# Optimization experiments

Hardware: AMD Instinct MI355X
Metric: run time of the kernel (lower is better)

## Reference

```python
import jax, jax.numpy as jnp
import numpy as np

N = 8192      # nodes
IN_FEATS = 128
OUT_FEATS = 64
DEG = 16      # avg degree for random edges
NEG_SLOPE = 0.01  # nn.LeakyReLU default


def setup_inputs() -> dict:
    key = jax.random.key(0)
    k1, k2, k3, k4, k5, k6 = jax.random.split(key, 6)
    inputs = jax.random.normal(k1, (N, IN_FEATS), dtype=jnp.float32)
    # Random symmetric adjacency with self-loops (dense, as in the original module)
    us = jax.random.randint(k2, (N * DEG,), 0, N)
    vs = jax.random.randint(k3, (N * DEG,), 0, N)
    A = jnp.zeros((N, N), dtype=jnp.float32)
    A = A.at[us, vs].set(1.0)
    A = A.at[vs, us].set(1.0)
    idx = jnp.arange(N)
    A = A.at[idx, idx].set(1.0)
    # Linear layer params (torch nn.Linear: weight [out, in])
    W = jax.random.normal(k4, (OUT_FEATS, IN_FEATS), dtype=jnp.float32) * (1.0 / np.sqrt(IN_FEATS))
    b = jnp.zeros((OUT_FEATS,), dtype=jnp.float32)
    # attention params, torch.rand -> uniform [0,1)
    a1 = jax.random.uniform(k5, (1, OUT_FEATS), dtype=jnp.float32)
    a2 = jax.random.uniform(k6, (1, OUT_FEATS), dtype=jnp.float32)
    return {"inputs": inputs, "A": A, "W": W, "b": b, "a1": a1, "a2": a2}


def reference(inputs, A, W, b, a1, a2):
    z = inputs @ W.T + b                                  # [N, out]
    zi = jnp.sum(a1 * z, axis=1, keepdims=True)           # [N, 1]
    zj = jnp.sum(a2 * z, axis=1, keepdims=True)           # [N, 1]
    n = A.shape[0]
    idx = jnp.arange(n)
    diagA = jnp.diagonal(A)                               # A_ii
    # attention_A + attention_B = A*zi + diag(A_ii * zj)  (A*(eye*zj) only keeps diagonal)
    att = A * zi
    att = att.at[idx, idx].add(diagA * zj[:, 0])
    att = jax.nn.leaky_relu(att, NEG_SLOPE)
    att = jnp.exp(att) * A
    att = att / jnp.sum(att, axis=1, keepdims=True)       # row-normalize
    h = z - att @ z
    return jax.nn.relu(h)
```

## Files before the change

kernel.cpp:

```cpp
#include <hip/hip_runtime.h>
#include <math.h>

#define NN 8192
#define IN_F 128
#define OUT_F 64
#define NEG_SLOPE 0.01f

__global__ __launch_bounds__(256) void k1_linear(
    const float* __restrict__ X, const float* __restrict__ W,
    const float* __restrict__ b, const float* __restrict__ a1,
    const float* __restrict__ a2, float* __restrict__ z,
    float* __restrict__ ev, float* __restrict__ dv)
{
    __shared__ float Wl[OUT_F * 129];
    __shared__ float xs[4 * IN_F];
    const int t = threadIdx.x;
    const int blk = blockIdx.x;

    for (int idx = t; idx < OUT_F * IN_F; idx += 256) {
        int f = idx >> 7, k = idx & 127;
        Wl[f * 129 + k] = W[idx];
    }
    for (int idx = t; idx < 4 * IN_F; idx += 256) {
        xs[idx] = X[(size_t)blk * (4 * IN_F) + idx];
    }
    __syncthreads();

    const int r = t >> 6;
    const int f = t & 63;
    float acc = 0.f;
#pragma unroll 8
    for (int k = 0; k < IN_F; ++k)
        acc = fmaf(xs[r * IN_F + k], Wl[f * 129 + k], acc);
    const float zval = acc + b[f];
    z[blk * 256 + t] = zval;

    float p1 = a1[f] * zval;
    float p2 = a2[f] * zval;
#pragma unroll
    for (int off = 32; off > 0; off >>= 1) {
        p1 += __shfl_down(p1, off, 64);
        p2 += __shfl_down(p2, off, 64);
    }
    if (f == 0) {
        const int i = blk * 4 + r;
        const float zi = p1, zj = p2;
        const float s1 = zi;
        const float s2 = zi + zj;
        const float l1 = s1 > 0.f ? s1 : NEG_SLOPE * s1;
        const float l2 = s2 > 0.f ? s2 : NEG_SLOPE * s2;
        ev[i] = expf(l1);
        dv[i] = expf(l2);
    }
}

__global__ __launch_bounds__(256) void k2_row(
    const float* __restrict__ A, const float* __restrict__ z,
    const float* __restrict__ ev, const float* __restrict__ dv,
    float* __restrict__ out)
{
    __shared__ int   list[1024];
    __shared__ int   cnt;
    __shared__ float accw[4][64];
    __shared__ float degw[4];

    const int i = blockIdx.x;
    const int t = threadIdx.x;
    const int wid = t >> 6, lane = t & 63;
    const float4* __restrict__ Arow =
        reinterpret_cast<const float4*>(A + (size_t)i * NN);

    float accReg = 0.f;
    float degLocal = 0.f;

    for (int c = 0; c < NN / 1024; ++c) {
        __syncthreads();
        if (t == 0) cnt = 0;
        __syncthreads();

        const float4 a4 = Arow[c * 256 + t];
        degLocal += a4.x + a4.y + a4.z + a4.w;
        const int j0 = c * 1024 + t * 4;
        if (a4.x != 0.f) list[atomicAdd(&cnt, 1)] = j0;
        if (a4.y != 0.f) list[atomicAdd(&cnt, 1)] = j0 + 1;
        if (a4.z != 0.f) list[atomicAdd(&cnt, 1)] = j0 + 2;
        if (a4.w != 0.f) list[atomicAdd(&cnt, 1)] = j0 + 3;
        __syncthreads();

        const int m = cnt;
        for (int base = 0; base < m; base += 4) {
            const int idx = base + wid;
            if (idx < m) {
                const int j = list[idx];
                accReg += z[j * 64 + lane];
            }
        }
    }

#pragma unroll
    for (int off = 32; off > 0; off >>= 1)
        degLocal += __shfl_down(degLocal, off, 64);
    if (lane == 0) degw[wid] = degLocal;
    accw[wid][lane] = accReg;
    __syncthreads();

    if (t < 64) {
        const float deg = degw[0] + degw[1] + degw[2] + degw[3];
        const float sumNbr = accw[0][t] + accw[1][t] + accw[2][t] + accw[3][t];
        const float e = ev[i], d = dv[i];
        const float S = (deg - 1.f) * e + d;
        const float zif = z[i * 64 + t];
        const float h = zif * (1.f + (e - d) / S) - (e / S) * sumNbr;
        out[(size_t)i * 64 + t] = h > 0.f ? h : 0.f;
    }
}

extern "C" void kernel_launch(void* const* d_in, const int* in_sizes, int n_in,
                              void* d_out, int out_size, void* d_ws, size_t ws_size,
                              hipStream_t stream) {
    const float* X  = (const float*)d_in[0];
    const float* A  = (const float*)d_in[1];
    const float* W  = (const float*)d_in[2];
    const float* b  = (const float*)d_in[3];
    const float* a1 = (const float*)d_in[4];
    const float* a2 = (const float*)d_in[5];
    float* out = (float*)d_out;

    float* ws = (float*)d_ws;
    float* z  = ws;
    float* ev = ws + NN * OUT_F;
    float* dv = ev + NN;

    k1_linear<<<NN / 4, 256, 0, stream>>>(X, W, b, a1, a2, z, ev, dv);
    k2_row<<<NN, 256, 0, stream>>>(A, z, ev, dv, out);
}
```

Baseline: 75.44 us.

## Replace shared-list neighbor compaction with wave ballots; batch rows per linear block

In the row kernel, the per-chunk shared-memory list built with atomics and block barriers is replaced by wave-level ballots. Each wave walks the set bits of its ballot masks to gather z rows directly. All eight float4 loads of a wave's A-row slice are issued up front into registers, so the barriers disappear and more loads are in flight. The linear kernel now handles 32 rows per block, which amortizes the shared W load over more rows, and it loads X with float4. The tradeoff is higher register pressure and serial per-wave gather loops.

```diff
diff --git a/kernel.cpp b/kernel.cpp
--- a/kernel.cpp
+++ b/kernel.cpp
@@ -5,6 +5,7 @@
 #define IN_F 128
 #define OUT_F 64
 #define NEG_SLOPE 0.01f
+#define K1_ROWS 32
 
 __global__ __launch_bounds__(256) void k1_linear(
     const float* __restrict__ X, const float* __restrict__ W,
@@ -13,7 +14,7 @@
     float* __restrict__ ev, float* __restrict__ dv)
 {
     __shared__ float Wl[OUT_F * 129];
-    __shared__ float xs[4 * IN_F];
+    __shared__ float xs[K1_ROWS * IN_F];
     const int t = threadIdx.x;
     const int blk = blockIdx.x;
 
@@ -21,36 +22,46 @@
         int f = idx >> 7, k = idx & 127;
         Wl[f * 129 + k] = W[idx];
     }
-    for (int idx = t; idx < 4 * IN_F; idx += 256) {
-        xs[idx] = X[(size_t)blk * (4 * IN_F) + idx];
+    {
+        const float4* Xv = reinterpret_cast<const float4*>(X + (size_t)blk * (K1_ROWS * IN_F));
+        float4* xsv = reinterpret_cast<float4*>(xs);
+#pragma unroll
+        for (int idx = t; idx < K1_ROWS * IN_F / 4; idx += 256)
+            xsv[idx] = Xv[idx];
     }
     __syncthreads();
 
-    const int r = t >> 6;
-    const int f = t & 63;
-    float acc = 0.f;
+    const int wid = t >> 6;
+    const int lane = t & 63;
+    const float bias = b[lane];
+    const float a1f = a1[lane], a2f = a2[lane];
+
+#pragma unroll
+    for (int r8 = 0; r8 < 8; ++r8) {
+        const int row = wid * 8 + r8;
+        float acc = 0.f;
 #pragma unroll 8
-    for (int k = 0; k < IN_F; ++k)
-        acc = fmaf(xs[r * IN_F + k], Wl[f * 129 + k], acc);
-    const float zval = acc + b[f];
-    z[blk * 256 + t] = zval;
+        for (int k = 0; k < IN_F; ++k)
+            acc = fmaf(xs[row * IN_F + k], Wl[lane * 129 + k], acc);
+        const float zval = acc + bias;
+        const int i = blk * K1_ROWS + row;
+        z[i * OUT_F + lane] = zval;
 
-    float p1 = a1[f] * zval;
-    float p2 = a2[f] * zval;
+        float p1 = a1f * zval;
+        float p2 = a2f * zval;
 #pragma unroll
-    for (int off = 32; off > 0; off >>= 1) {
-        p1 += __shfl_down(p1, off, 64);
-        p2 += __shfl_down(p2, off, 64);
-    }
-    if (f == 0) {
-        const int i = blk * 4 + r;
-        const float zi = p1, zj = p2;
-        const float s1 = zi;
-        const float s2 = zi + zj;
-        const float l1 = s1 > 0.f ? s1 : NEG_SLOPE * s1;
-        const float l2 = s2 > 0.f ? s2 : NEG_SLOPE * s2;
-        ev[i] = expf(l1);
-        dv[i] = expf(l2);
+        for (int off = 32; off > 0; off >>= 1) {
+            p1 += __shfl_down(p1, off, 64);
+            p2 += __shfl_down(p2, off, 64);
+        }
+        if (lane == 0) {
+            const float s1 = p1;
+            const float s2 = p1 + p2;
+            const float l1 = s1 > 0.f ? s1 : NEG_SLOPE * s1;
+            const float l2 = s2 > 0.f ? s2 : NEG_SLOPE * s2;
+            ev[i] = expf(l1);
+            dv[i] = expf(l2);
+        }
     }
 }
 
@@ -59,8 +70,6 @@
     const float* __restrict__ ev, const float* __restrict__ dv,
     float* __restrict__ out)
 {
-    __shared__ int   list[1024];
-    __shared__ int   cnt;
     __shared__ float accw[4][64];
     __shared__ float degw[4];
 
@@ -70,48 +79,49 @@
     const float4* __restrict__ Arow =
         reinterpret_cast<const float4*>(A + (size_t)i * NN);
 
-    float accReg = 0.f;
-    float degLocal = 0.f;
+    float4 v[8];
+#pragma unroll
+    for (int c = 0; c < 8; ++c)
+        v[c] = Arow[wid * 512 + c * 64 + lane];
 
-    for (int c = 0; c < NN / 1024; ++c) {
-        __syncthreads();
-        if (t == 0) cnt = 0;
-        __syncthreads();
+    float acc = 0.f;
+    float deg = 0.f;
 
-        const float4 a4 = Arow[c * 256 + t];
-        degLocal += a4.x + a4.y + a4.z + a4.w;
-        const int j0 = c * 1024 + t * 4;
-        if (a4.x != 0.f) list[atomicAdd(&cnt, 1)] = j0;
-        if (a4.y != 0.f) list[atomicAdd(&cnt, 1)] = j0 + 1;
-        if (a4.z != 0.f) list[atomicAdd(&cnt, 1)] = j0 + 2;
-        if (a4.w != 0.f) list[atomicAdd(&cnt, 1)] = j0 + 3;
-        __syncthreads();
-
-        const int m = cnt;
-        for (int base = 0; base < m; base += 4) {
-            const int idx = base + wid;
-            if (idx < m) {
-                const int j = list[idx];
-                accReg += z[j * 64 + lane];
-            }
-        }
+#pragma unroll
+    for (int c = 0; c < 8; ++c) {
+        const float4 a4 = v[c];
+        deg += a4.x + a4.y + a4.z + a4.w;
+        const int jbase = wid * 2048 + c * 256;
+        unsigned long long m;
+        m = __ballot(a4.x != 0.f);
+        while (m) { int l = __builtin_ctzll(m); m &= m - 1;
+                    acc += z[(size_t)(jbase + l * 4 + 0) * OUT_F + lane]; }
+        m = __ballot(a4.y != 0.f);
+        while (m) { int l = __builtin_ctzll(m); m &= m - 1;
+                    acc += z[(size_t)(jbase + l * 4 + 1) * OUT_F + lane]; }
+        m = __ballot(a4.z != 0.f);
+        while (m) { int l = __builtin_ctzll(m); m &= m - 1;
+                    acc += z[(size_t)(jbase + l * 4 + 2) * OUT_F + lane]; }
+        m = __ballot(a4.w != 0.f);
+        while (m) { int l = __builtin_ctzll(m); m &= m - 1;
+                    acc += z[(size_t)(jbase + l * 4 + 3) * OUT_F + lane]; }
     }
 
 #pragma unroll
     for (int off = 32; off > 0; off >>= 1)
-        degLocal += __shfl_down(degLocal, off, 64);
-    if (lane == 0) degw[wid] = degLocal;
-    accw[wid][lane] = accReg;
+        deg += __shfl_down(deg, off, 64);
+    if (lane == 0) degw[wid] = deg;
+    accw[wid][lane] = acc;
     __syncthreads();
 
     if (t < 64) {
-        const float deg = degw[0] + degw[1] + degw[2] + degw[3];
+        const float degT = degw[0] + degw[1] + degw[2] + degw[3];
         const float sumNbr = accw[0][t] + accw[1][t] + accw[2][t] + accw[3][t];
         const float e = ev[i], d = dv[i];
-        const float S = (deg - 1.f) * e + d;
-        const float zif = z[i * 64 + t];
+        const float S = (degT - 1.f) * e + d;
+        const float zif = z[(size_t)i * OUT_F + t];
         const float h = zif * (1.f + (e - d) / S) - (e / S) * sumNbr;
-        out[(size_t)i * 64 + t] = h > 0.f ? h : 0.f;
+        out[(size_t)i * OUT_F + t] = h > 0.f ? h : 0.f;
     }
 }
 
@@ -131,6 +141,6 @@
     float* ev = ws + NN * OUT_F;
     float* dv = ev + NN;
 
-    k1_linear<<<NN / 4, 256, 0, stream>>>(X, W, b, a1, a2, z, ev, dv);
+    k1_linear<<<NN / K1_ROWS, 256, 0, stream>>>(X, W, b, a1, a2, z, ev, dv);
     k2_row<<<NN, 256, 0, stream>>>(A, z, ev, dv, out);
 }
```

Result: faster. 72.12 us (-4.4%).
